# Performance work log

Measured on AMD Instinct MI355X. Metric: run time of the kernel, lower is better.

## Reference

```python
import jax, jax.numpy as jnp
import numpy as np

P = 22536   # priors
B = 32      # batch
M = 16      # objects per image (fixed for jit)
C = 81      # classes incl. background
THRESHOLD = 0.5
ALPHA_REG = 1.0   # config.reg_weights
FL_ALPHA = 0.25
FL_GAMMA = 2.0
EPS = 1e-7


def cxcy_to_xy(c):
    return jnp.concatenate([c[..., :2] - c[..., 2:] / 2, c[..., :2] + c[..., 2:] / 2], -1)


def gcxgcy_to_cxcy(g, p):
    return jnp.concatenate([g[..., :2] * p[..., 2:] / 10 + p[..., :2],
                            jnp.exp(g[..., 2:] / 5) * p[..., 2:]], -1)


def iou_xy(a, b):
    # a: (M,4) xyxy, b: (P,4) xyxy -> (M,P)
    lt = jnp.maximum(a[:, None, :2], b[None, :, :2])
    rb = jnp.minimum(a[:, None, 2:], b[None, :, 2:])
    inter = jnp.prod(jnp.clip(rb - lt, 0.0), -1)
    area_a = jnp.prod(a[:, 2:] - a[:, :2], -1)
    area_b = jnp.prod(b[:, 2:] - b[:, :2], -1)
    return inter / (area_a[:, None] + area_b[None, :] - inter)


def diou_loss(p, g):
    # elementwise DIoU loss, p/g: (..., 4) xyxy -> (...)
    lt = jnp.maximum(p[..., :2], g[..., :2])
    rb = jnp.minimum(p[..., 2:], g[..., 2:])
    inter = jnp.prod(jnp.clip(rb - lt, 0.0), -1)
    ap = jnp.prod(p[..., 2:] - p[..., :2], -1)
    ag = jnp.prod(g[..., 2:] - g[..., :2], -1)
    iou = inter / (ap + ag - inter + EPS)
    cp = (p[..., :2] + p[..., 2:]) / 2
    cg = (g[..., :2] + g[..., 2:]) / 2
    d2 = jnp.sum((cp - cg) ** 2, -1)
    elt = jnp.minimum(p[..., :2], g[..., :2])
    erb = jnp.maximum(p[..., 2:], g[..., 2:])
    c2 = jnp.sum((erb - elt) ** 2, -1) + EPS
    return 1.0 - iou + d2 / c2


def match_image(boxes_i, labels_i, priors_xy):
    # boxes_i: (M,4), labels_i: (M,), priors_xy: (P,4)
    overlap = iou_xy(boxes_i, priors_xy)                 # (M,P)
    ofp = overlap.max(0)                                  # overlap_for_each_prior (P,)
    obj = jnp.argmax(overlap, 0)                          # object_for_each_prior (P,)
    pfo = jnp.argmax(overlap, 1)                          # prior_for_each_object (M,)
    obj = obj.at[pfo].set(jnp.arange(M))
    ofp = ofp.at[pfo].set(1.0)
    lab = labels_i[obj]                                   # (P,)
    lab_neg = jnp.where(ofp < THRESHOLD - 0.1, -1, lab)
    lab = jnp.where(ofp < THRESHOLD, 0, lab)
    true_locs = boxes_i[obj]                              # (P,4)
    return lab, lab_neg, true_locs


def setup_inputs() -> dict:
    key = jax.random.key(0)
    k1, k2, k3, k4, k5, k6, k7 = jax.random.split(key, 7)
    pcxy = jax.random.uniform(k1, (P, 2), minval=0.05, maxval=0.95)
    pwh = jax.random.uniform(k2, (P, 2), minval=0.02, maxval=0.3)
    priors_cxcy = jnp.concatenate([pcxy, pwh], -1)
    ctr = jax.random.uniform(k3, (B, M, 2), minval=0.2, maxval=0.8)
    wh = jax.random.uniform(k4, (B, M, 2), minval=0.05, maxval=0.3)
    boxes = jnp.concatenate([ctr - wh / 2, ctr + wh / 2], -1)
    labels = jax.random.randint(k5, (B, M), 1, C).astype(jnp.int32)
    predicted_locs = jax.random.normal(k6, (B, P, 4), dtype=jnp.float32)
    predicted_scores = jax.random.normal(k7, (B, P, C), dtype=jnp.float32)
    return {"predicted_locs": predicted_locs, "predicted_scores": predicted_scores,
            "boxes": boxes, "labels": labels, "priors_cxcy": priors_cxcy}


def reference(predicted_locs, predicted_scores, boxes, labels, priors_cxcy):
    priors_xy = cxcy_to_xy(priors_cxcy)
    lab, lab_neg, true_locs = jax.vmap(match_image, in_axes=(0, 0, None))(boxes, labels, priors_xy)
    decoded = cxcy_to_xy(gcxgcy_to_cxcy(predicted_locs, priors_cxcy))   # (B,P,4)
    pos = lab > 0
    neg = lab_neg == -1
    # DIoU localization loss, mean over positive priors
    loc = diou_loss(decoded, true_locs)                                 # (B,P)
    npos = jnp.maximum(pos.sum(), 1)
    loc_loss = jnp.sum(loc * pos) / npos
    # focal classification loss over union of positive and hard-negative priors
    logp = jax.nn.log_softmax(predicted_scores, -1)                     # (B,P,C)
    lp_t = jnp.take_along_axis(logp, lab[..., None], -1)[..., 0]        # (B,P)
    pt = jnp.exp(lp_t)
    fl = FL_ALPHA * (1.0 - pt) ** FL_GAMMA * (-lp_t)
    m = pos | neg
    conf_loss = jnp.sum(fl * m) / jnp.maximum(m.sum(), 1)
    return conf_loss + ALPHA_REG * loc_loss
```

## Files before the change

kernel.cpp:

```cpp
#include <hip/hip_runtime.h>

#define PN 22536
#define BN 32
#define MN 16
#define CN 81

__global__ __launch_bounds__(256)
void match_kernel(const float* __restrict__ boxes,
                  const float* __restrict__ priors,
                  float* __restrict__ ofp,
                  int* __restrict__ obj,
                  unsigned long long* __restrict__ pfo_key)
{
    const int b = blockIdx.y;
    const int p = blockIdx.x * 256 + threadIdx.x;

    __shared__ float4 sbox[MN];
    __shared__ float  sarea[MN];
    if (threadIdx.x < MN) {
        float4 bx = reinterpret_cast<const float4*>(boxes)[b * MN + threadIdx.x];
        sbox[threadIdx.x]  = bx;
        sarea[threadIdx.x] = (bx.z - bx.x) * (bx.w - bx.y);
    }
    __syncthreads();

    float x0 = 0.f, y0 = 0.f, x1 = 0.f, y1 = 0.f, ab = 0.f;
    const bool valid = (p < PN);
    if (valid) {
        float4 pc = reinterpret_cast<const float4*>(priors)[p];
        float hw = pc.z / 2.0f, hh = pc.w / 2.0f;
        x0 = pc.x - hw; y0 = pc.y - hh;
        x1 = pc.x + hw; y1 = pc.y + hh;
        ab = (x1 - x0) * (y1 - y0);
    }

    float iou_m[MN];
    float best = -1.0f;
    int bestm = 0;
    #pragma unroll
    for (int m = 0; m < MN; ++m) {
        float iou = 0.0f;
        if (valid) {
            float4 bx = sbox[m];
            float lx = fmaxf(bx.x, x0), ly = fmaxf(bx.y, y0);
            float rx = fminf(bx.z, x1), ry = fminf(bx.w, y1);
            float inter = fmaxf(rx - lx, 0.0f) * fmaxf(ry - ly, 0.0f);
            iou = inter / (sarea[m] + ab - inter);
        }
        iou_m[m] = iou;
        if (iou > best) { best = iou; bestm = m; }
    }
    if (valid) {
        ofp[b * PN + p] = best;
        obj[b * PN + p] = bestm;
    }

    const int lane = threadIdx.x & 63;
    #pragma unroll
    for (int m = 0; m < MN; ++m) {
        unsigned long long key =
            ((unsigned long long)__float_as_uint(iou_m[m]) << 32) |
            (unsigned long long)(~(unsigned int)p);
        #pragma unroll
        for (int off = 32; off >= 1; off >>= 1) {
            unsigned long long o = __shfl_down(key, (unsigned)off, 64);
            if (o > key) key = o;
        }
        if (lane == 0) atomicMax(&pfo_key[b * MN + m], key);
    }
}

__global__ void scatter_kernel(const unsigned long long* __restrict__ pfo_key,
                               float* __restrict__ ofp, int* __restrict__ obj)
{
    int b = threadIdx.x;
    if (b >= BN) return;
    for (int m = 0; m < MN; ++m) {
        unsigned int low = (unsigned int)pfo_key[b * MN + m];
        int p = (int)(~low);
        obj[b * PN + p] = m;
        ofp[b * PN + p] = 1.0f;
    }
}

__global__ __launch_bounds__(256)
void loss_kernel(const float* __restrict__ plocs,
                 const float* __restrict__ scores,
                 const float* __restrict__ boxes,
                 const int*   __restrict__ labels,
                 const float* __restrict__ priors,
                 const float* __restrict__ ofp,
                 const int*   __restrict__ obj,
                 float* __restrict__ partials)
{
    const int tid = blockIdx.x * 256 + threadIdx.x;
    const int stride = gridDim.x * 256;
    const int R = BN * PN;

    float conf_acc = 0.f, m_cnt = 0.f, loc_acc = 0.f, pos_cnt = 0.f;

    for (int row = tid; row < R; row += stride) {
        float ofp_v = ofp[row];
        bool pos = ofp_v >= 0.5f;
        bool neg = ofp_v < 0.4f;
        if (!(pos || neg)) continue;

        const float* srow = scores + (size_t)row * CN;
        float r[CN];
        #pragma unroll
        for (int i = 0; i < CN; ++i) r[i] = srow[i];

        float mx = r[0];
        #pragma unroll
        for (int i = 1; i < CN; ++i) mx = fmaxf(mx, r[i]);

        float se = 0.f;
        #pragma unroll
        for (int i = 0; i < CN; ++i) se += expf(r[i] - mx);

        int b = row / PN;
        int obj_v = obj[row];
        int lab = pos ? labels[b * MN + obj_v] : 0;
        float s_lab = srow[lab];
        float lp = s_lab - mx - logf(se);
        float pt = expf(lp);
        float om = 1.0f - pt;
        conf_acc += 0.25f * om * om * (-lp);
        m_cnt += 1.0f;

        if (pos) {
            int p = row - b * PN;
            float4 g  = reinterpret_cast<const float4*>(plocs)[row];
            float4 pc = reinterpret_cast<const float4*>(priors)[p];
            float cx = g.x * pc.z / 10.0f + pc.x;
            float cy = g.y * pc.w / 10.0f + pc.y;
            float w  = expf(g.z / 5.0f) * pc.z;
            float h  = expf(g.w / 5.0f) * pc.w;
            float px0 = cx - w / 2.0f, py0 = cy - h / 2.0f;
            float px1 = cx + w / 2.0f, py1 = cy + h / 2.0f;

            float4 gb = reinterpret_cast<const float4*>(boxes)[b * MN + obj_v];
            float lx = fmaxf(px0, gb.x), ly = fmaxf(py0, gb.y);
            float rx = fminf(px1, gb.z), ry = fminf(py1, gb.w);
            float inter = fmaxf(rx - lx, 0.f) * fmaxf(ry - ly, 0.f);
            float ap = (px1 - px0) * (py1 - py0);
            float ag = (gb.z - gb.x) * (gb.w - gb.y);
            float iou = inter / (ap + ag - inter + 1e-7f);
            float cpx = (px0 + px1) / 2.0f, cpy = (py0 + py1) / 2.0f;
            float cgx = (gb.x + gb.z) / 2.0f, cgy = (gb.y + gb.w) / 2.0f;
            float dx = cpx - cgx, dy = cpy - cgy;
            float d2 = dx * dx + dy * dy;
            float ex0 = fminf(px0, gb.x), ey0 = fminf(py0, gb.y);
            float ex1 = fmaxf(px1, gb.z), ey1 = fmaxf(py1, gb.w);
            float ew = ex1 - ex0, eh = ey1 - ey0;
            float c2 = ew * ew + eh * eh + 1e-7f;
            loc_acc += 1.0f - iou + d2 / c2;
            pos_cnt += 1.0f;
        }
    }

    #pragma unroll
    for (int off = 32; off >= 1; off >>= 1) {
        conf_acc += __shfl_down(conf_acc, (unsigned)off, 64);
        m_cnt    += __shfl_down(m_cnt,    (unsigned)off, 64);
        loc_acc  += __shfl_down(loc_acc,  (unsigned)off, 64);
        pos_cnt  += __shfl_down(pos_cnt,  (unsigned)off, 64);
    }
    __shared__ float sred[4][4];
    const int lane = threadIdx.x & 63;
    const int w = threadIdx.x >> 6;
    if (lane == 0) {
        sred[w][0] = conf_acc; sred[w][1] = m_cnt;
        sred[w][2] = loc_acc;  sred[w][3] = pos_cnt;
    }
    __syncthreads();
    if (threadIdx.x == 0) {
        float a = 0.f, bsum = 0.f, c = 0.f, d = 0.f;
        #pragma unroll
        for (int i = 0; i < 4; ++i) {
            a += sred[i][0]; bsum += sred[i][1];
            c += sred[i][2]; d += sred[i][3];
        }
        partials[blockIdx.x * 4 + 0] = a;
        partials[blockIdx.x * 4 + 1] = bsum;
        partials[blockIdx.x * 4 + 2] = c;
        partials[blockIdx.x * 4 + 3] = d;
    }
}

__global__ __launch_bounds__(256)
void reduce_kernel(const float* __restrict__ partials, int nblk,
                   float* __restrict__ out)
{
    float c = 0.f, mc = 0.f, l = 0.f, pc = 0.f;
    for (int i = threadIdx.x; i < nblk; i += 256) {
        c  += partials[i * 4 + 0];
        mc += partials[i * 4 + 1];
        l  += partials[i * 4 + 2];
        pc += partials[i * 4 + 3];
    }
    #pragma unroll
    for (int off = 32; off >= 1; off >>= 1) {
        c  += __shfl_down(c,  (unsigned)off, 64);
        mc += __shfl_down(mc, (unsigned)off, 64);
        l  += __shfl_down(l,  (unsigned)off, 64);
        pc += __shfl_down(pc, (unsigned)off, 64);
    }
    __shared__ float s[4][4];
    int lane = threadIdx.x & 63, w = threadIdx.x >> 6;
    if (lane == 0) { s[w][0] = c; s[w][1] = mc; s[w][2] = l; s[w][3] = pc; }
    __syncthreads();
    if (threadIdx.x == 0) {
        float C = 0.f, Mc = 0.f, L = 0.f, Pc = 0.f;
        for (int i = 0; i < 4; ++i) {
            C += s[i][0]; Mc += s[i][1]; L += s[i][2]; Pc += s[i][3];
        }
        out[0] = C / fmaxf(Mc, 1.0f) + L / fmaxf(Pc, 1.0f);
    }
}

extern "C" void kernel_launch(void* const* d_in, const int* in_sizes, int n_in,
                              void* d_out, int out_size, void* d_ws, size_t ws_size,
                              hipStream_t stream)
{
    const float* plocs  = (const float*)d_in[0];
    const float* scores = (const float*)d_in[1];
    const float* boxes  = (const float*)d_in[2];
    const int*   labels = (const int*)d_in[3];
    const float* priors = (const float*)d_in[4];
    float* out = (float*)d_out;

    char* ws = (char*)d_ws;
    unsigned long long* pfo_key = (unsigned long long*)ws;
    float* ofp = (float*)(ws + 4096);
    int*   obj = (int*)(ws + 4096 + (size_t)BN * PN * 4);
    float* partials = (float*)(ws + 4096 + 2 * (size_t)BN * PN * 4);

    hipMemsetAsync(pfo_key, 0, BN * MN * sizeof(unsigned long long), stream);

    dim3 gA((PN + 255) / 256, BN);
    match_kernel<<<gA, 256, 0, stream>>>(boxes, priors, ofp, obj, pfo_key);
    scatter_kernel<<<1, 64, 0, stream>>>(pfo_key, ofp, obj);

    const int NBLK = 1024;
    loss_kernel<<<NBLK, 256, 0, stream>>>(plocs, scores, boxes, labels, priors,
                                          ofp, obj, partials);
    reduce_kernel<<<1, 256, 0, stream>>>(partials, NBLK, out);
}
```

Baseline: 444.9 us.

## Fuse matching into loss kernel with wave-per-row softmax and recomputed IoU

Drops the ofp/obj intermediate arrays and the scatter kernel. The loss kernel now recomputes per-prior IoU argmax from shared-memory boxes and applies the prior-for-object override through a ballot. Each 64-lane wave handles one score row with coalesced lane loads and shuffle reductions, replacing the old per-thread 81-element row loads that were strided and uncoalesced. The pfo kernel also pre-reduces its atomics in shared memory. In exchange, the IoU work is done twice and lanes sit idle on the serial lane-0 tail.

Result: slower. 537.8 us (+20.9%).

```diff
diff --git a/kernel.cpp b/kernel.cpp
--- a/kernel.cpp
+++ b/kernel.cpp
@@ -1,26 +1,29 @@
 #include <hip/hip_runtime.h>
+#include <math.h>
 
 #define PN 22536
 #define BN 32
 #define MN 16
 #define CN 81
+#define NBX 177
+#define LOSS_ITERS 32
 
 __global__ __launch_bounds__(256)
-void match_kernel(const float* __restrict__ boxes,
-                  const float* __restrict__ priors,
-                  float* __restrict__ ofp,
-                  int* __restrict__ obj,
-                  unsigned long long* __restrict__ pfo_key)
+void pfo_kernel(const float* __restrict__ boxes,
+                const float* __restrict__ priors,
+                unsigned long long* __restrict__ pfo_key)
 {
     const int b = blockIdx.y;
     const int p = blockIdx.x * 256 + threadIdx.x;
 
     __shared__ float4 sbox[MN];
     __shared__ float  sarea[MN];
+    __shared__ unsigned long long skey[MN];
     if (threadIdx.x < MN) {
         float4 bx = reinterpret_cast<const float4*>(boxes)[b * MN + threadIdx.x];
         sbox[threadIdx.x]  = bx;
         sarea[threadIdx.x] = (bx.z - bx.x) * (bx.w - bx.y);
+        skey[threadIdx.x]  = 0ull;
     }
     __syncthreads();
 
@@ -34,53 +37,29 @@
         ab = (x1 - x0) * (y1 - y0);
     }
 
-    float iou_m[MN];
-    float best = -1.0f;
-    int bestm = 0;
+    const int lane = threadIdx.x & 63;
     #pragma unroll
     for (int m = 0; m < MN; ++m) {
-        float iou = 0.0f;
+        unsigned long long key = 0ull;
         if (valid) {
             float4 bx = sbox[m];
             float lx = fmaxf(bx.x, x0), ly = fmaxf(bx.y, y0);
             float rx = fminf(bx.z, x1), ry = fminf(bx.w, y1);
             float inter = fmaxf(rx - lx, 0.0f) * fmaxf(ry - ly, 0.0f);
-            iou = inter / (sarea[m] + ab - inter);
-        }
-        iou_m[m] = iou;
-        if (iou > best) { best = iou; bestm = m; }
-    }
-    if (valid) {
-        ofp[b * PN + p] = best;
-        obj[b * PN + p] = bestm;
-    }
-
-    const int lane = threadIdx.x & 63;
-    #pragma unroll
-    for (int m = 0; m < MN; ++m) {
-        unsigned long long key =
-            ((unsigned long long)__float_as_uint(iou_m[m]) << 32) |
-            (unsigned long long)(~(unsigned int)p);
+            float iou = inter / (sarea[m] + ab - inter);
+            key = ((unsigned long long)__float_as_uint(iou) << 32) |
+                  (unsigned long long)(~(unsigned int)p);
+        }
         #pragma unroll
         for (int off = 32; off >= 1; off >>= 1) {
             unsigned long long o = __shfl_down(key, (unsigned)off, 64);
             if (o > key) key = o;
         }
-        if (lane == 0) atomicMax(&pfo_key[b * MN + m], key);
-    }
-}
-
-__global__ void scatter_kernel(const unsigned long long* __restrict__ pfo_key,
-                               float* __restrict__ ofp, int* __restrict__ obj)
-{
-    int b = threadIdx.x;
-    if (b >= BN) return;
-    for (int m = 0; m < MN; ++m) {
-        unsigned int low = (unsigned int)pfo_key[b * MN + m];
-        int p = (int)(~low);
-        obj[b * PN + p] = m;
-        ofp[b * PN + p] = 1.0f;
-    }
+        if (lane == 0) atomicMax(&skey[m], key);
+    }
+    __syncthreads();
+    if (threadIdx.x < MN)
+        atomicMax(&pfo_key[b * MN + threadIdx.x], skey[threadIdx.x]);
 }
 
 __global__ __launch_bounds__(256)
@@ -89,122 +68,155 @@
                  const float* __restrict__ boxes,
                  const int*   __restrict__ labels,
                  const float* __restrict__ priors,
-                 const float* __restrict__ ofp,
-                 const int*   __restrict__ obj,
+                 const unsigned long long* __restrict__ pfo_key,
                  float* __restrict__ partials)
 {
-    const int tid = blockIdx.x * 256 + threadIdx.x;
-    const int stride = gridDim.x * 256;
-    const int R = BN * PN;
+    const int b    = blockIdx.y;
+    const int w    = threadIdx.x >> 6;
+    const int lane = threadIdx.x & 63;
+
+    __shared__ float4 sbox[MN];
+    __shared__ float  sarea[MN];
+    __shared__ int    slab[MN];
+    __shared__ int    spfo[MN];
+    __shared__ float  sred[4][4];
+
+    if (threadIdx.x < MN) {
+        float4 bx = reinterpret_cast<const float4*>(boxes)[b * MN + threadIdx.x];
+        sbox[threadIdx.x]  = bx;
+        sarea[threadIdx.x] = (bx.z - bx.x) * (bx.w - bx.y);
+        slab[threadIdx.x]  = labels[b * MN + threadIdx.x];
+        spfo[threadIdx.x]  = (int)(~(unsigned int)(pfo_key[b * MN + threadIdx.x] &
+                                                   0xFFFFFFFFull));
+    }
+    __syncthreads();
 
     float conf_acc = 0.f, m_cnt = 0.f, loc_acc = 0.f, pos_cnt = 0.f;
 
-    for (int row = tid; row < R; row += stride) {
-        float ofp_v = ofp[row];
-        bool pos = ofp_v >= 0.5f;
-        bool neg = ofp_v < 0.4f;
+    for (int it = 0; it < LOSS_ITERS; ++it) {
+        const int p = it * (NBX * 4) + blockIdx.x * 4 + w;
+        if (p >= PN) break;
+
+        float4 pc = reinterpret_cast<const float4*>(priors)[p];
+        float hw = pc.z / 2.0f, hh = pc.w / 2.0f;
+        float qx0 = pc.x - hw, qy0 = pc.y - hh;
+        float qx1 = pc.x + hw, qy1 = pc.y + hh;
+        float ab  = (qx1 - qx0) * (qy1 - qy0);
+
+        unsigned long long key = 0ull;
+        if (lane < MN) {
+            float4 bx = sbox[lane];
+            float lx = fmaxf(bx.x, qx0), ly = fmaxf(bx.y, qy0);
+            float rx = fminf(bx.z, qx1), ry = fminf(bx.w, qy1);
+            float inter = fmaxf(rx - lx, 0.0f) * fmaxf(ry - ly, 0.0f);
+            float iou = inter / (sarea[lane] + ab - inter);
+            key = ((unsigned long long)__float_as_uint(iou) << 32) |
+                  (unsigned long long)(~(unsigned int)lane);
+        }
+        #pragma unroll
+        for (int off = 1; off < 64; off <<= 1) {
+            unsigned long long o = __shfl_xor(key, off, 64);
+            if (o > key) key = o;
+        }
+        int   bestm = (int)(~(unsigned int)(key & 0xFFFFFFFFull));
+        float ofp   = __uint_as_float((unsigned int)(key >> 32));
+
+        bool pm = (lane < MN) && (spfo[lane] == p);
+        unsigned long long mask = __ballot(pm);
+        if (mask) { bestm = 63 - __clzll(mask); ofp = 1.0f; }
+
+        bool pos = ofp >= 0.5f;
+        bool neg = ofp < 0.4f;
         if (!(pos || neg)) continue;
 
-        const float* srow = scores + (size_t)row * CN;
-        float r[CN];
-        #pragma unroll
-        for (int i = 0; i < CN; ++i) r[i] = srow[i];
-
-        float mx = r[0];
-        #pragma unroll
-        for (int i = 1; i < CN; ++i) mx = fmaxf(mx, r[i]);
-
-        float se = 0.f;
-        #pragma unroll
-        for (int i = 0; i < CN; ++i) se += expf(r[i] - mx);
-
-        int b = row / PN;
-        int obj_v = obj[row];
-        int lab = pos ? labels[b * MN + obj_v] : 0;
-        float s_lab = srow[lab];
-        float lp = s_lab - mx - logf(se);
-        float pt = expf(lp);
-        float om = 1.0f - pt;
-        conf_acc += 0.25f * om * om * (-lp);
-        m_cnt += 1.0f;
-
-        if (pos) {
-            int p = row - b * PN;
-            float4 g  = reinterpret_cast<const float4*>(plocs)[row];
-            float4 pc = reinterpret_cast<const float4*>(priors)[p];
-            float cx = g.x * pc.z / 10.0f + pc.x;
-            float cy = g.y * pc.w / 10.0f + pc.y;
-            float w  = expf(g.z / 5.0f) * pc.z;
-            float h  = expf(g.w / 5.0f) * pc.w;
-            float px0 = cx - w / 2.0f, py0 = cy - h / 2.0f;
-            float px1 = cx + w / 2.0f, py1 = cy + h / 2.0f;
-
-            float4 gb = reinterpret_cast<const float4*>(boxes)[b * MN + obj_v];
-            float lx = fmaxf(px0, gb.x), ly = fmaxf(py0, gb.y);
-            float rx = fminf(px1, gb.z), ry = fminf(py1, gb.w);
-            float inter = fmaxf(rx - lx, 0.f) * fmaxf(ry - ly, 0.f);
-            float ap = (px1 - px0) * (py1 - py0);
-            float ag = (gb.z - gb.x) * (gb.w - gb.y);
-            float iou = inter / (ap + ag - inter + 1e-7f);
-            float cpx = (px0 + px1) / 2.0f, cpy = (py0 + py1) / 2.0f;
-            float cgx = (gb.x + gb.z) / 2.0f, cgy = (gb.y + gb.w) / 2.0f;
-            float dx = cpx - cgx, dy = cpy - cgy;
-            float d2 = dx * dx + dy * dy;
-            float ex0 = fminf(px0, gb.x), ey0 = fminf(py0, gb.y);
-            float ex1 = fmaxf(px1, gb.z), ey1 = fmaxf(py1, gb.w);
-            float ew = ex1 - ex0, eh = ey1 - ey0;
-            float c2 = ew * ew + eh * eh + 1e-7f;
-            loc_acc += 1.0f - iou + d2 / c2;
-            pos_cnt += 1.0f;
-        }
-    }
-
-    #pragma unroll
-    for (int off = 32; off >= 1; off >>= 1) {
-        conf_acc += __shfl_down(conf_acc, (unsigned)off, 64);
-        m_cnt    += __shfl_down(m_cnt,    (unsigned)off, 64);
-        loc_acc  += __shfl_down(loc_acc,  (unsigned)off, 64);
-        pos_cnt  += __shfl_down(pos_cnt,  (unsigned)off, 64);
-    }
-    __shared__ float sred[4][4];
-    const int lane = threadIdx.x & 63;
-    const int w = threadIdx.x >> 6;
+        const float* srow = scores + ((size_t)b * PN + p) * CN;
+        float r0 = srow[lane];
+        float r1 = (lane < CN - 64) ? srow[64 + lane] : -INFINITY;
+
+        float mx = fmaxf(r0, r1);
+        #pragma unroll
+        for (int off = 1; off < 64; off <<= 1)
+            mx = fmaxf(mx, __shfl_xor(mx, off, 64));
+
+        float es = expf(r0 - mx) + ((lane < CN - 64) ? expf(r1 - mx) : 0.0f);
+        #pragma unroll
+        for (int off = 1; off < 64; off <<= 1)
+            es += __shfl_xor(es, off, 64);
+
+        int lab = pos ? slab[bestm] : 0;
+        float tv;
+        if (lab < 64) tv = __shfl(r0, lab, 64);
+        else          tv = __shfl(r1, lab - 64, 64);
+
+        if (lane == 0) {
+            float lp = tv - mx - logf(es);
+            float pt = expf(lp);
+            float om = 1.0f - pt;
+            conf_acc += 0.25f * om * om * (-lp);
+            m_cnt += 1.0f;
+
+            if (pos) {
+                float4 g = reinterpret_cast<const float4*>(plocs)[(size_t)b * PN + p];
+                float cx = g.x * pc.z / 10.0f + pc.x;
+                float cy = g.y * pc.w / 10.0f + pc.y;
+                float ww = expf(g.z / 5.0f) * pc.z;
+                float hh2 = expf(g.w / 5.0f) * pc.w;
+                float px0 = cx - ww / 2.0f, py0 = cy - hh2 / 2.0f;
+                float px1 = cx + ww / 2.0f, py1 = cy + hh2 / 2.0f;
+
+                float4 gb = sbox[bestm];
+                float lx = fmaxf(px0, gb.x), ly = fmaxf(py0, gb.y);
+                float rx = fminf(px1, gb.z), ry = fminf(py1, gb.w);
+                float inter = fmaxf(rx - lx, 0.f) * fmaxf(ry - ly, 0.f);
+                float apx = (px1 - px0) * (py1 - py0);
+                float agx = (gb.z - gb.x) * (gb.w - gb.y);
+                float iou = inter / (apx + agx - inter + 1e-7f);
+                float cpx = (px0 + px1) / 2.0f, cpy = (py0 + py1) / 2.0f;
+                float cgx = (gb.x + gb.z) / 2.0f, cgy = (gb.y + gb.w) / 2.0f;
+                float dx = cpx - cgx, dy = cpy - cgy;
+                float d2 = dx * dx + dy * dy;
+                float ex0 = fminf(px0, gb.x), ey0 = fminf(py0, gb.y);
+                float ex1 = fmaxf(px1, gb.z), ey1 = fmaxf(py1, gb.w);
+                float ew = ex1 - ex0, eh = ey1 - ey0;
+                float c2 = ew * ew + eh * eh + 1e-7f;
+                loc_acc += 1.0f - iou + d2 / c2;
+                pos_cnt += 1.0f;
+            }
+        }
+    }
+
     if (lane == 0) {
         sred[w][0] = conf_acc; sred[w][1] = m_cnt;
         sred[w][2] = loc_acc;  sred[w][3] = pos_cnt;
     }
     __syncthreads();
     if (threadIdx.x == 0) {
-        float a = 0.f, bsum = 0.f, c = 0.f, d = 0.f;
+        float a = 0.f, bs = 0.f, c = 0.f, d = 0.f;
         #pragma unroll
         for (int i = 0; i < 4; ++i) {
-            a += sred[i][0]; bsum += sred[i][1];
+            a += sred[i][0]; bs += sred[i][1];
             c += sred[i][2]; d += sred[i][3];
         }
-        partials[blockIdx.x * 4 + 0] = a;
-        partials[blockIdx.x * 4 + 1] = bsum;
-        partials[blockIdx.x * 4 + 2] = c;
-        partials[blockIdx.x * 4 + 3] = d;
+        float4* po = reinterpret_cast<float4*>(partials);
+        po[b * NBX + blockIdx.x] = make_float4(a, bs, c, d);
     }
 }
 
 __global__ __launch_bounds__(256)
-void reduce_kernel(const float* __restrict__ partials, int nblk,
-                   float* __restrict__ out)
-{
+void reduce_kernel(const float* __restrict__ partials, float* __restrict__ out)
+{
+    const int N = BN * NBX;
     float c = 0.f, mc = 0.f, l = 0.f, pc = 0.f;
-    for (int i = threadIdx.x; i < nblk; i += 256) {
-        c  += partials[i * 4 + 0];
-        mc += partials[i * 4 + 1];
-        l  += partials[i * 4 + 2];
-        pc += partials[i * 4 + 3];
+    for (int i = threadIdx.x; i < N; i += 256) {
+        float4 v = reinterpret_cast<const float4*>(partials)[i];
+        c += v.x; mc += v.y; l += v.z; pc += v.w;
     }
     #pragma unroll
-    for (int off = 32; off >= 1; off >>= 1) {
-        c  += __shfl_down(c,  (unsigned)off, 64);
-        mc += __shfl_down(mc, (unsigned)off, 64);
-        l  += __shfl_down(l,  (unsigned)off, 64);
-        pc += __shfl_down(pc, (unsigned)off, 64);
+    for (int off = 1; off < 64; off <<= 1) {
+        c  += __shfl_xor(c,  off, 64);
+        mc += __shfl_xor(mc, off, 64);
+        l  += __shfl_xor(l,  off, 64);
+        pc += __shfl_xor(pc, off, 64);
     }
     __shared__ float s[4][4];
     int lane = threadIdx.x & 63, w = threadIdx.x >> 6;
@@ -212,6 +224,7 @@
     __syncthreads();
     if (threadIdx.x == 0) {
         float C = 0.f, Mc = 0.f, L = 0.f, Pc = 0.f;
+        #pragma unroll
         for (int i = 0; i < 4; ++i) {
             C += s[i][0]; Mc += s[i][1]; L += s[i][2]; Pc += s[i][3];
         }
@@ -232,18 +245,15 @@
 
     char* ws = (char*)d_ws;
     unsigned long long* pfo_key = (unsigned long long*)ws;
-    float* ofp = (float*)(ws + 4096);
-    int*   obj = (int*)(ws + 4096 + (size_t)BN * PN * 4);
-    float* partials = (float*)(ws + 4096 + 2 * (size_t)BN * PN * 4);
+    float* partials = (float*)(ws + 4096);
 
     hipMemsetAsync(pfo_key, 0, BN * MN * sizeof(unsigned long long), stream);
 
     dim3 gA((PN + 255) / 256, BN);
-    match_kernel<<<gA, 256, 0, stream>>>(boxes, priors, ofp, obj, pfo_key);
-    scatter_kernel<<<1, 64, 0, stream>>>(pfo_key, ofp, obj);
-
-    const int NBLK = 1024;
-    loss_kernel<<<NBLK, 256, 0, stream>>>(plocs, scores, boxes, labels, priors,
-                                          ofp, obj, partials);
-    reduce_kernel<<<1, 256, 0, stream>>>(partials, NBLK, out);
-}
+    pfo_kernel<<<gA, 256, 0, stream>>>(boxes, priors, pfo_key);
+
+    dim3 gB(NBX, BN);
+    loss_kernel<<<gB, 256, 0, stream>>>(plocs, scores, boxes, labels, priors,
+                                        pfo_key, partials);
+    reduce_kernel<<<1, 256, 0, stream>>>(partials, out);
+}
```
